# Optimization experiments

Hardware: AMD Instinct MI355X
Metric: run time of the kernel (lower is better)

Reference implementation:

```python
import jax, jax.numpy as jnp
import numpy as np

N_NODES = 100000
N_EDGES = 1600000
D = 128
LN_EPS = 1e-5


def setup_inputs() -> dict:
    key = jax.random.key(0)
    ks = jax.random.split(key, 6)
    return {
        "x": jax.random.normal(ks[0], (N_NODES, D), dtype=jnp.float32),
        "edge_src": jax.random.randint(ks[1], (N_EDGES,), 0, N_NODES, dtype=jnp.int32),
        "edge_dst": jax.random.randint(ks[2], (N_EDGES,), 0, N_NODES, dtype=jnp.int32),
        "edge_val": jax.random.uniform(ks[3], (N_EDGES,), dtype=jnp.float32),
        "w1": jax.random.normal(ks[4], (D,), dtype=jnp.float32),
        "w2": jax.random.normal(ks[5], (D,), dtype=jnp.float32),
        "ln1_g": jnp.ones((D,), dtype=jnp.float32),
        "ln1_b": jnp.zeros((D,), dtype=jnp.float32),
        "ln2_g": jnp.ones((D,), dtype=jnp.float32),
        "ln2_b": jnp.zeros((D,), dtype=jnp.float32),
    }


def _layer_norm(x, g, b):
    mu = jnp.mean(x, axis=-1, keepdims=True)
    var = jnp.mean(jnp.square(x - mu), axis=-1, keepdims=True)
    return (x - mu) * jax.lax.rsqrt(var + LN_EPS) * g + b


def _gat_layer(x, w, src, dst, val, g, b):
    # diag transform: h = x * w  (elementwise over features)
    h = x * w
    # sparse adjacency aggregation: out[dst] += val * h[src]
    msg = val[:, None] * h[src]  # [E, D]
    out = jax.ops.segment_sum(msg, dst, num_segments=x.shape[0])
    return _layer_norm(out, g, b)


def reference(x, edge_src, edge_dst, edge_val, w1, w2, ln1_g, ln1_b, ln2_g, ln2_b):
    # layer 0 (followed by ReLU; dropout is identity in eval mode)
    h = _gat_layer(x, w1, edge_src, edge_dst, edge_val, ln1_g, ln1_b)
    h = jax.nn.relu(h)
    # layer 1 (last layer: no ReLU/dropout)
    out = _gat_layer(h, w2, edge_src, edge_dst, edge_val, ln2_g, ln2_b)
    return out
```

## Files before the change

### kernel.cpp

```cpp
#include <hip/hip_runtime.h>

#define D 128
#define LN_EPS 1e-5f
#define BUCKET_NODES 128
#define BUCKET_SHIFT 7
#define EDGE_CAP 4096
#define FUSE_THREADS 512
#define K2_EPT 16
#define SORT_THREADS 512
#define SORT_EPT 8

__device__ inline unsigned int pack_b2(float a, float b) {
    unsigned ua = __float_as_uint(a);
    unsigned ub = __float_as_uint(b);
    unsigned pa = (ua + 0x7fffu + ((ua >> 16) & 1u)) >> 16;
    unsigned pb = (ub + 0x7fffu + ((ub >> 16) & 1u)) & 0xffff0000u;
    return pa | pb;
}
__device__ inline float lo_b2(unsigned u) { return __uint_as_float((u & 0xffffu) << 16); }
__device__ inline float hi_b2(unsigned u) { return __uint_as_float(u & 0xffff0000u); }

__global__ __launch_bounds__(FUSE_THREADS)
void conv_fill_kernel(const float* __restrict__ x, unsigned int* __restrict__ xb,
                      int nwords, int conv_blocks,
                      const int* __restrict__ src, const int* __restrict__ dst,
                      const float* __restrict__ val,
                      int* __restrict__ gcnt, uint2* __restrict__ edges,
                      int E, int nbuckets) {
    if ((int)blockIdx.x < conv_blocks) {
        int i = blockIdx.x * FUSE_THREADS + threadIdx.x;
        if (i < nwords) {
            int node = i >> 6, f = i & 63;
            xb[i] = pack_b2(x[(size_t)node * D + f], x[(size_t)node * D + 64 + f]);
        }
        return;
    }
    __shared__ int lcnt[1024];
    __shared__ int lbase[1024];
    int fb = (int)blockIdx.x - conv_blocks;
    for (int i = threadIdx.x; i < nbuckets; i += FUSE_THREADS) lcnt[i] = 0;
    __syncthreads();

    int base = fb * (FUSE_THREADS * K2_EPT);
    unsigned int w0[K2_EPT];
    float        w1[K2_EPT];
    int          br[K2_EPT];
    #pragma unroll
    for (int r = 0; r < K2_EPT; ++r) {
        int e = base + r * FUSE_THREADS + threadIdx.x;
        if (e < E) {
            int d = dst[e];
            int b = d >> BUCKET_SHIFT;
            int rk = atomicAdd(&lcnt[b], 1);
            w0[r] = (unsigned)src[e] | ((unsigned)(d & (BUCKET_NODES - 1)) << 20);
            w1[r] = val[e];
            br[r] = (b << 16) | rk;
        } else {
            br[r] = -1;
        }
    }
    __syncthreads();
    for (int i = threadIdx.x; i < nbuckets; i += FUSE_THREADS) {
        int c = lcnt[i];
        lbase[i] = c ? atomicAdd(&gcnt[i], c) : 0;
    }
    __syncthreads();
    #pragma unroll
    for (int r = 0; r < K2_EPT; ++r) {
        if (br[r] >= 0) {
            int b  = br[r] >> 16;
            int rk = br[r] & 0xffff;
            edges[(size_t)b * EDGE_CAP + lbase[b] + rk] =
                make_uint2(w0[r], __float_as_uint(w1[r]));
        }
    }
}

__global__ __launch_bounds__(SORT_THREADS)
void bucket_sort_kernel(uint2* __restrict__ edges,
                        const int* __restrict__ gcnt,
                        int* __restrict__ deg,
                        int* __restrict__ offsets,
                        int N) {
    __shared__ int hist[BUCKET_NODES];
    __shared__ int scan[BUCKET_NODES];
    int b = blockIdx.x;
    int cnt = gcnt[b];
    uint2* ep = edges + (size_t)b * EDGE_CAP;

    if (threadIdx.x < BUCKET_NODES) hist[threadIdx.x] = 0;
    __syncthreads();

    uint2 ed[SORT_EPT];
    int   rk[SORT_EPT];
    int   dl[SORT_EPT];
    #pragma unroll
    for (int r = 0; r < SORT_EPT; ++r) {
        int i = r * SORT_THREADS + threadIdx.x;
        if (i < cnt) {
            uint2 t = ep[i];
            int d = (int)(t.x >> 20);
            ed[r] = t;
            dl[r] = d;
            rk[r] = atomicAdd(&hist[d], 1);
        } else {
            dl[r] = -1;
        }
    }
    __syncthreads();

    if (threadIdx.x < BUCKET_NODES) scan[threadIdx.x] = hist[threadIdx.x];
    __syncthreads();
    #pragma unroll
    for (int off = 1; off < BUCKET_NODES; off <<= 1) {
        int v = 0;
        if (threadIdx.x < BUCKET_NODES && threadIdx.x >= off) v = scan[threadIdx.x - off];
        __syncthreads();
        if (threadIdx.x < BUCKET_NODES) scan[threadIdx.x] += v;
        __syncthreads();
    }

    int node0 = b << BUCKET_SHIFT;
    if (threadIdx.x < BUCKET_NODES) {
        int n = node0 + threadIdx.x;
        if (n < N) {
            deg[n]     = hist[threadIdx.x];
            offsets[n] = b * EDGE_CAP + scan[threadIdx.x] - hist[threadIdx.x];
        }
    }
    __syncthreads();

    #pragma unroll
    for (int r = 0; r < SORT_EPT; ++r) {
        if (dl[r] >= 0) {
            int p = scan[dl[r]] - hist[dl[r]] + rk[r];
            ep[p] = ed[r];
        }
    }
}

__global__ void gather_ln_kernel(const unsigned int* __restrict__ h2,
                                 const int* __restrict__ offsets,
                                 const int* __restrict__ deg,
                                 const uint2* __restrict__ edge_s,
                                 const float* __restrict__ w,
                                 const float* __restrict__ g,
                                 const float* __restrict__ bb,
                                 float* __restrict__ out_f32,
                                 unsigned int* __restrict__ out_b2,
                                 int N, int mode) {
    int node = blockIdx.x * (blockDim.x >> 6) + (threadIdx.x >> 6);
    int lane = threadIdx.x & 63;
    if (node >= N) return;

    int q  = lane >> 4;
    int sl = lane & 15;

    int start = offsets[node];
    int cnt   = deg[node];

    const uint4* h4 = (const uint4*)h2;
    float aA0 = 0.f, aA1 = 0.f, aA2 = 0.f, aA3 = 0.f;
    float aB0 = 0.f, aB1 = 0.f, aB2 = 0.f, aB3 = 0.f;

    for (int base = 0; base < cnt; base += 64) {
        int m = min(64, cnt - base);
        unsigned e0 = 0u, e1 = 0u;
        if (lane < m) { uint2 t = edge_s[start + base + lane]; e0 = t.x; e1 = t.y; }
        for (int j = 0; j < m; j += 4) {
            int idx = j + q;
            int   s = __shfl((int)e0, idx, 64) & 0xfffff;
            float v = __uint_as_float((unsigned)__shfl((int)e1, idx, 64));
            uint4 hw = h4[(size_t)s * 16 + sl];
            aA0 = fmaf(v, lo_b2(hw.x), aA0);  aB0 = fmaf(v, hi_b2(hw.x), aB0);
            aA1 = fmaf(v, lo_b2(hw.y), aA1);  aB1 = fmaf(v, hi_b2(hw.y), aB1);
            aA2 = fmaf(v, lo_b2(hw.z), aA2);  aB2 = fmaf(v, hi_b2(hw.z), aB2);
            aA3 = fmaf(v, lo_b2(hw.w), aA3);  aB3 = fmaf(v, hi_b2(hw.w), aB3);
        }
    }

    aA0 += __shfl_xor(aA0, 16, 64); aA0 += __shfl_xor(aA0, 32, 64);
    aA1 += __shfl_xor(aA1, 16, 64); aA1 += __shfl_xor(aA1, 32, 64);
    aA2 += __shfl_xor(aA2, 16, 64); aA2 += __shfl_xor(aA2, 32, 64);
    aA3 += __shfl_xor(aA3, 16, 64); aA3 += __shfl_xor(aA3, 32, 64);
    aB0 += __shfl_xor(aB0, 16, 64); aB0 += __shfl_xor(aB0, 32, 64);
    aB1 += __shfl_xor(aB1, 16, 64); aB1 += __shfl_xor(aB1, 32, 64);
    aB2 += __shfl_xor(aB2, 16, 64); aB2 += __shfl_xor(aB2, 32, 64);
    aB3 += __shfl_xor(aB3, 16, 64); aB3 += __shfl_xor(aB3, 32, 64);

    float4 wA = ((const float4*)w)[sl];
    float4 wB = ((const float4*)(w + 64))[sl];
    aA0 *= wA.x; aA1 *= wA.y; aA2 *= wA.z; aA3 *= wA.w;
    aB0 *= wB.x; aB1 *= wB.y; aB2 *= wB.z; aB3 *= wB.w;

    float sum = ((aA0 + aA1) + (aA2 + aA3)) + ((aB0 + aB1) + (aB2 + aB3));
    sum += __shfl_xor(sum, 1, 64); sum += __shfl_xor(sum, 2, 64);
    sum += __shfl_xor(sum, 4, 64); sum += __shfl_xor(sum, 8, 64);
    float mu = sum * (1.0f / D);

    float dA0 = aA0 - mu, dA1 = aA1 - mu, dA2 = aA2 - mu, dA3 = aA3 - mu;
    float dB0 = aB0 - mu, dB1 = aB1 - mu, dB2 = aB2 - mu, dB3 = aB3 - mu;
    float sq = ((dA0*dA0 + dA1*dA1) + (dA2*dA2 + dA3*dA3))
             + ((dB0*dB0 + dB1*dB1) + (dB2*dB2 + dB3*dB3));
    sq += __shfl_xor(sq, 1, 64); sq += __shfl_xor(sq, 2, 64);
    sq += __shfl_xor(sq, 4, 64); sq += __shfl_xor(sq, 8, 64);
    float rstd = rsqrtf(sq * (1.0f / D) + LN_EPS);

    float4 gA = ((const float4*)g)[sl];
    float4 gB = ((const float4*)(g + 64))[sl];
    float4 bA = ((const float4*)bb)[sl];
    float4 bB = ((const float4*)(bb + 64))[sl];
    float oA0 = dA0 * rstd * gA.x + bA.x, oA1 = dA1 * rstd * gA.y + bA.y;
    float oA2 = dA2 * rstd * gA.z + bA.z, oA3 = dA3 * rstd * gA.w + bA.w;
    float oB0 = dB0 * rstd * gB.x + bB.x, oB1 = dB1 * rstd * gB.y + bB.y;
    float oB2 = dB2 * rstd * gB.z + bB.z, oB3 = dB3 * rstd * gB.w + bB.w;

    if (mode == 1) {
        oA0 = fmaxf(oA0, 0.f); oA1 = fmaxf(oA1, 0.f);
        oA2 = fmaxf(oA2, 0.f); oA3 = fmaxf(oA3, 0.f);
        oB0 = fmaxf(oB0, 0.f); oB1 = fmaxf(oB1, 0.f);
        oB2 = fmaxf(oB2, 0.f); oB3 = fmaxf(oB3, 0.f);
        if (q == 0) {
            uint4 pw;
            pw.x = pack_b2(oA0, oB0); pw.y = pack_b2(oA1, oB1);
            pw.z = pack_b2(oA2, oB2); pw.w = pack_b2(oA3, oB3);
            ((uint4*)(out_b2 + (size_t)node * 64))[sl] = pw;
        }
    } else {
        if (q == 0) {
            ((float4*)(out_f32 + (size_t)node * D))[sl]      = make_float4(oA0, oA1, oA2, oA3);
            ((float4*)(out_f32 + (size_t)node * D + 64))[sl] = make_float4(oB0, oB1, oB2, oB3);
        }
    }
}

extern "C" void kernel_launch(void* const* d_in, const int* in_sizes, int n_in,
                              void* d_out, int out_size, void* d_ws, size_t ws_size,
                              hipStream_t stream) {
    const float* x    = (const float*)d_in[0];
    const int*   esrc = (const int*)d_in[1];
    const int*   edst = (const int*)d_in[2];
    const float* eval_= (const float*)d_in[3];
    const float* w1   = (const float*)d_in[4];
    const float* w2   = (const float*)d_in[5];
    const float* g1   = (const float*)d_in[6];
    const float* b1   = (const float*)d_in[7];
    const float* g2   = (const float*)d_in[8];
    const float* b2   = (const float*)d_in[9];
    float* out = (float*)d_out;

    const int N = in_sizes[0] / D;
    const int E = in_sizes[1];
    const int nbuckets = (N + BUCKET_NODES - 1) >> BUCKET_SHIFT;

    unsigned int* xb      = (unsigned int*)d_ws;
    unsigned int* hb      = xb + (size_t)N * 64;
    uint2*        edges   = (uint2*)(hb + (size_t)N * 64);
    int*          gcnt    = (int*)(edges + (size_t)nbuckets * EDGE_CAP);
    int*          deg     = gcnt + nbuckets;
    int*          offsets = deg + N;

    const int nwords = N * 64;
    const int conv_blocks = (nwords + FUSE_THREADS - 1) / FUSE_THREADS;
    const int fill_blocks = (E + FUSE_THREADS * K2_EPT - 1) / (FUSE_THREADS * K2_EPT);
    const int ggrid = (N + 3) / 4;

    hipMemsetAsync(gcnt, 0, (size_t)nbuckets * sizeof(int), stream);
    conv_fill_kernel<<<conv_blocks + fill_blocks, FUSE_THREADS, 0, stream>>>(
        x, xb, nwords, conv_blocks, esrc, edst, eval_, gcnt, edges, E, nbuckets);
    bucket_sort_kernel<<<nbuckets, SORT_THREADS, 0, stream>>>(edges, gcnt,
                                                              deg, offsets, N);
    gather_ln_kernel<<<ggrid, 256, 0, stream>>>(xb, offsets, deg, edges,
                                                w1, g1, b1, nullptr, hb, N, 1);
    gather_ln_kernel<<<ggrid, 256, 0, stream>>>(hb, offsets, deg, edges,
                                                w2, g2, b2, out, nullptr, N, 0);
}
```

Before: 308.5 us.

## Fuse bucket sort into gather kernel via LDS sorting, switch to fp16 features

Removes the separate bucket-sort kernel and the deg/offsets arrays. Each gather block now owns one 128-node bucket, sorts that bucket's edges in shared memory, and then has each 16-lane group aggregate whole nodes with two independent loads in flight per iteration. Feature storage moves from bf16 to fp16 packing via cvt_pkrtz. In exchange, the sort is redone in both layers, and 1024-thread blocks with a 32KB LDS buffer may lower occupancy. fp16 also has narrower range than bf16, and cvt_pkrtz rounds toward zero.

```diff
diff --git a/kernel.cpp b/kernel.cpp
--- a/kernel.cpp
+++ b/kernel.cpp
@@ -1,4 +1,6 @@
 #include <hip/hip_runtime.h>
+
+typedef __fp16 half2_t __attribute__((ext_vector_type(2)));
 
 #define D 128
 #define LN_EPS 1e-5f
@@ -7,18 +9,12 @@
 #define EDGE_CAP 4096
 #define FUSE_THREADS 512
 #define K2_EPT 16
-#define SORT_THREADS 512
-#define SORT_EPT 8
-
-__device__ inline unsigned int pack_b2(float a, float b) {
-    unsigned ua = __float_as_uint(a);
-    unsigned ub = __float_as_uint(b);
-    unsigned pa = (ua + 0x7fffu + ((ua >> 16) & 1u)) >> 16;
-    unsigned pb = (ub + 0x7fffu + ((ub >> 16) & 1u)) & 0xffff0000u;
-    return pa | pb;
-}
-__device__ inline float lo_b2(unsigned u) { return __uint_as_float((u & 0xffffu) << 16); }
-__device__ inline float hi_b2(unsigned u) { return __uint_as_float(u & 0xffff0000u); }
+#define GT 1024
+
+__device__ inline unsigned pack_h2(float a, float b) {
+    half2_t p = __builtin_amdgcn_cvt_pkrtz(a, b);
+    return __builtin_bit_cast(unsigned, p);
+}
 
 __global__ __launch_bounds__(FUSE_THREADS)
 void conv_fill_kernel(const float* __restrict__ x, unsigned int* __restrict__ xb,
@@ -31,7 +27,7 @@
         int i = blockIdx.x * FUSE_THREADS + threadIdx.x;
         if (i < nwords) {
             int node = i >> 6, f = i & 63;
-            xb[i] = pack_b2(x[(size_t)node * D + f], x[(size_t)node * D + 64 + f]);
+            xb[i] = pack_h2(x[(size_t)node * D + f], x[(size_t)node * D + 64 + f]);
         }
         return;
     }
@@ -76,160 +72,136 @@
     }
 }
 
-__global__ __launch_bounds__(SORT_THREADS)
-void bucket_sort_kernel(uint2* __restrict__ edges,
-                        const int* __restrict__ gcnt,
-                        int* __restrict__ deg,
-                        int* __restrict__ offsets,
-                        int N) {
+__global__ __launch_bounds__(GT, 8)
+void gather_ln_kernel(const uint4* __restrict__ h4,
+                      const int* __restrict__ gcnt,
+                      const uint2* __restrict__ edges_g,
+                      const float* __restrict__ w,
+                      const float* __restrict__ g,
+                      const float* __restrict__ bb,
+                      float* __restrict__ out_f32,
+                      unsigned int* __restrict__ out_h,
+                      int N, int mode) {
+    __shared__ uint2 eL[EDGE_CAP];
     __shared__ int hist[BUCKET_NODES];
-    __shared__ int scan[BUCKET_NODES];
-    int b = blockIdx.x;
-    int cnt = gcnt[b];
-    uint2* ep = edges + (size_t)b * EDGE_CAP;
-
-    if (threadIdx.x < BUCKET_NODES) hist[threadIdx.x] = 0;
-    __syncthreads();
-
-    uint2 ed[SORT_EPT];
-    int   rk[SORT_EPT];
-    int   dl[SORT_EPT];
-    #pragma unroll
-    for (int r = 0; r < SORT_EPT; ++r) {
-        int i = r * SORT_THREADS + threadIdx.x;
+    __shared__ int scanb[BUCKET_NODES];
+    __shared__ int obase[BUCKET_NODES];
+
+    int bkt = blockIdx.x;
+    int tid = threadIdx.x;
+    int cnt = min(gcnt[bkt], EDGE_CAP);
+    const uint2* ep = edges_g + (size_t)bkt * EDGE_CAP;
+
+    if (tid < BUCKET_NODES) hist[tid] = 0;
+    __syncthreads();
+
+    uint2 ed[4]; int dl[4]; int rk[4];
+    #pragma unroll
+    for (int r = 0; r < 4; ++r) {
+        int i = r * GT + tid;
         if (i < cnt) {
             uint2 t = ep[i];
-            int d = (int)(t.x >> 20);
             ed[r] = t;
-            dl[r] = d;
-            rk[r] = atomicAdd(&hist[d], 1);
-        } else {
-            dl[r] = -1;
-        }
-    }
-    __syncthreads();
-
-    if (threadIdx.x < BUCKET_NODES) scan[threadIdx.x] = hist[threadIdx.x];
+            dl[r] = (int)(t.x >> 20);
+            rk[r] = atomicAdd(&hist[dl[r]], 1);
+        } else dl[r] = -1;
+    }
+    __syncthreads();
+    if (tid < BUCKET_NODES) scanb[tid] = hist[tid];
     __syncthreads();
     #pragma unroll
     for (int off = 1; off < BUCKET_NODES; off <<= 1) {
         int v = 0;
-        if (threadIdx.x < BUCKET_NODES && threadIdx.x >= off) v = scan[threadIdx.x - off];
+        if (tid < BUCKET_NODES && tid >= off) v = scanb[tid - off];
         __syncthreads();
-        if (threadIdx.x < BUCKET_NODES) scan[threadIdx.x] += v;
+        if (tid < BUCKET_NODES) scanb[tid] += v;
         __syncthreads();
     }
-
-    int node0 = b << BUCKET_SHIFT;
-    if (threadIdx.x < BUCKET_NODES) {
-        int n = node0 + threadIdx.x;
-        if (n < N) {
-            deg[n]     = hist[threadIdx.x];
-            offsets[n] = b * EDGE_CAP + scan[threadIdx.x] - hist[threadIdx.x];
-        }
-    }
-    __syncthreads();
-
-    #pragma unroll
-    for (int r = 0; r < SORT_EPT; ++r) {
-        if (dl[r] >= 0) {
-            int p = scan[dl[r]] - hist[dl[r]] + rk[r];
-            ep[p] = ed[r];
-        }
-    }
-}
-
-__global__ void gather_ln_kernel(const unsigned int* __restrict__ h2,
-                                 const int* __restrict__ offsets,
-                                 const int* __restrict__ deg,
-                                 const uint2* __restrict__ edge_s,
-                                 const float* __restrict__ w,
-                                 const float* __restrict__ g,
-                                 const float* __restrict__ bb,
-                                 float* __restrict__ out_f32,
-                                 unsigned int* __restrict__ out_b2,
-                                 int N, int mode) {
-    int node = blockIdx.x * (blockDim.x >> 6) + (threadIdx.x >> 6);
-    int lane = threadIdx.x & 63;
-    if (node >= N) return;
-
-    int q  = lane >> 4;
-    int sl = lane & 15;
-
-    int start = offsets[node];
-    int cnt   = deg[node];
-
-    const uint4* h4 = (const uint4*)h2;
-    float aA0 = 0.f, aA1 = 0.f, aA2 = 0.f, aA3 = 0.f;
-    float aB0 = 0.f, aB1 = 0.f, aB2 = 0.f, aB3 = 0.f;
-
-    for (int base = 0; base < cnt; base += 64) {
-        int m = min(64, cnt - base);
-        unsigned e0 = 0u, e1 = 0u;
-        if (lane < m) { uint2 t = edge_s[start + base + lane]; e0 = t.x; e1 = t.y; }
-        for (int j = 0; j < m; j += 4) {
-            int idx = j + q;
-            int   s = __shfl((int)e0, idx, 64) & 0xfffff;
-            float v = __uint_as_float((unsigned)__shfl((int)e1, idx, 64));
-            uint4 hw = h4[(size_t)s * 16 + sl];
-            aA0 = fmaf(v, lo_b2(hw.x), aA0);  aB0 = fmaf(v, hi_b2(hw.x), aB0);
-            aA1 = fmaf(v, lo_b2(hw.y), aA1);  aB1 = fmaf(v, hi_b2(hw.y), aB1);
-            aA2 = fmaf(v, lo_b2(hw.z), aA2);  aB2 = fmaf(v, hi_b2(hw.z), aB2);
-            aA3 = fmaf(v, lo_b2(hw.w), aA3);  aB3 = fmaf(v, hi_b2(hw.w), aB3);
-        }
-    }
-
-    aA0 += __shfl_xor(aA0, 16, 64); aA0 += __shfl_xor(aA0, 32, 64);
-    aA1 += __shfl_xor(aA1, 16, 64); aA1 += __shfl_xor(aA1, 32, 64);
-    aA2 += __shfl_xor(aA2, 16, 64); aA2 += __shfl_xor(aA2, 32, 64);
-    aA3 += __shfl_xor(aA3, 16, 64); aA3 += __shfl_xor(aA3, 32, 64);
-    aB0 += __shfl_xor(aB0, 16, 64); aB0 += __shfl_xor(aB0, 32, 64);
-    aB1 += __shfl_xor(aB1, 16, 64); aB1 += __shfl_xor(aB1, 32, 64);
-    aB2 += __shfl_xor(aB2, 16, 64); aB2 += __shfl_xor(aB2, 32, 64);
-    aB3 += __shfl_xor(aB3, 16, 64); aB3 += __shfl_xor(aB3, 32, 64);
+    if (tid < BUCKET_NODES) obase[tid] = scanb[tid] - hist[tid];
+    __syncthreads();
+    #pragma unroll
+    for (int r = 0; r < 4; ++r)
+        if (dl[r] >= 0) eL[obase[dl[r]] + rk[r]] = ed[r];
+    __syncthreads();
+
+    int wid = tid >> 6, lane = tid & 63, grp = lane >> 4, sl = lane & 15;
 
     float4 wA = ((const float4*)w)[sl];
     float4 wB = ((const float4*)(w + 64))[sl];
-    aA0 *= wA.x; aA1 *= wA.y; aA2 *= wA.z; aA3 *= wA.w;
-    aB0 *= wB.x; aB1 *= wB.y; aB2 *= wB.z; aB3 *= wB.w;
-
-    float sum = ((aA0 + aA1) + (aA2 + aA3)) + ((aB0 + aB1) + (aB2 + aB3));
-    sum += __shfl_xor(sum, 1, 64); sum += __shfl_xor(sum, 2, 64);
-    sum += __shfl_xor(sum, 4, 64); sum += __shfl_xor(sum, 8, 64);
-    float mu = sum * (1.0f / D);
-
-    float dA0 = aA0 - mu, dA1 = aA1 - mu, dA2 = aA2 - mu, dA3 = aA3 - mu;
-    float dB0 = aB0 - mu, dB1 = aB1 - mu, dB2 = aB2 - mu, dB3 = aB3 - mu;
-    float sq = ((dA0*dA0 + dA1*dA1) + (dA2*dA2 + dA3*dA3))
-             + ((dB0*dB0 + dB1*dB1) + (dB2*dB2 + dB3*dB3));
-    sq += __shfl_xor(sq, 1, 64); sq += __shfl_xor(sq, 2, 64);
-    sq += __shfl_xor(sq, 4, 64); sq += __shfl_xor(sq, 8, 64);
-    float rstd = rsqrtf(sq * (1.0f / D) + LN_EPS);
-
     float4 gA = ((const float4*)g)[sl];
     float4 gB = ((const float4*)(g + 64))[sl];
     float4 bA = ((const float4*)bb)[sl];
     float4 bB = ((const float4*)(bb + 64))[sl];
-    float oA0 = dA0 * rstd * gA.x + bA.x, oA1 = dA1 * rstd * gA.y + bA.y;
-    float oA2 = dA2 * rstd * gA.z + bA.z, oA3 = dA3 * rstd * gA.w + bA.w;
-    float oB0 = dB0 * rstd * gB.x + bB.x, oB1 = dB1 * rstd * gB.y + bB.y;
-    float oB2 = dB2 * rstd * gB.z + bB.z, oB3 = dB3 * rstd * gB.w + bB.w;
-
-    if (mode == 1) {
-        oA0 = fmaxf(oA0, 0.f); oA1 = fmaxf(oA1, 0.f);
-        oA2 = fmaxf(oA2, 0.f); oA3 = fmaxf(oA3, 0.f);
-        oB0 = fmaxf(oB0, 0.f); oB1 = fmaxf(oB1, 0.f);
-        oB2 = fmaxf(oB2, 0.f); oB3 = fmaxf(oB3, 0.f);
-        if (q == 0) {
+
+    #pragma unroll
+    for (int k = 0; k < 2; ++k) {
+        int ni = k * 64 + wid * 4 + grp;
+        int n = (bkt << BUCKET_SHIFT) + ni;
+        if (n >= N) continue;
+        int st = obase[ni], m = hist[ni];
+
+        float aA0=0,aA1=0,aA2=0,aA3=0, aB0=0,aB1=0,aB2=0,aB3=0;
+        for (int j = 0; j < m; j += 2) {
+            uint2 tA = eL[st + j];
+            uint2 tB = (j + 1 < m) ? eL[st + j + 1] : make_uint2(0u, 0u);
+            int   sA = (int)(tA.x & 0xfffffu);
+            float vA = __uint_as_float(tA.y);
+            int   sB = (int)(tB.x & 0xfffffu);
+            float vB = __uint_as_float(tB.y);
+            uint4 hA = h4[(size_t)sA * 16 + sl];
+            uint4 hB = h4[(size_t)sB * 16 + sl];
+            half2_t p;
+            p = __builtin_bit_cast(half2_t, hA.x);
+            aA0 = fmaf(vA, (float)p.x, aA0); aB0 = fmaf(vA, (float)p.y, aB0);
+            p = __builtin_bit_cast(half2_t, hA.y);
+            aA1 = fmaf(vA, (float)p.x, aA1); aB1 = fmaf(vA, (float)p.y, aB1);
+            p = __builtin_bit_cast(half2_t, hA.z);
+            aA2 = fmaf(vA, (float)p.x, aA2); aB2 = fmaf(vA, (float)p.y, aB2);
+            p = __builtin_bit_cast(half2_t, hA.w);
+            aA3 = fmaf(vA, (float)p.x, aA3); aB3 = fmaf(vA, (float)p.y, aB3);
+            p = __builtin_bit_cast(half2_t, hB.x);
+            aA0 = fmaf(vB, (float)p.x, aA0); aB0 = fmaf(vB, (float)p.y, aB0);
+            p = __builtin_bit_cast(half2_t, hB.y);
+            aA1 = fmaf(vB, (float)p.x, aA1); aB1 = fmaf(vB, (float)p.y, aB1);
+            p = __builtin_bit_cast(half2_t, hB.z);
+            aA2 = fmaf(vB, (float)p.x, aA2); aB2 = fmaf(vB, (float)p.y, aB2);
+            p = __builtin_bit_cast(half2_t, hB.w);
+            aA3 = fmaf(vB, (float)p.x, aA3); aB3 = fmaf(vB, (float)p.y, aB3);
+        }
+
+        aA0 *= wA.x; aA1 *= wA.y; aA2 *= wA.z; aA3 *= wA.w;
+        aB0 *= wB.x; aB1 *= wB.y; aB2 *= wB.z; aB3 *= wB.w;
+
+        float sum = ((aA0 + aA1) + (aA2 + aA3)) + ((aB0 + aB1) + (aB2 + aB3));
+        sum += __shfl_xor(sum, 1, 64); sum += __shfl_xor(sum, 2, 64);
+        sum += __shfl_xor(sum, 4, 64); sum += __shfl_xor(sum, 8, 64);
+        float mu = sum * (1.0f / D);
+
+        float dA0 = aA0 - mu, dA1 = aA1 - mu, dA2 = aA2 - mu, dA3 = aA3 - mu;
+        float dB0 = aB0 - mu, dB1 = aB1 - mu, dB2 = aB2 - mu, dB3 = aB3 - mu;
+        float sq = ((dA0*dA0 + dA1*dA1) + (dA2*dA2 + dA3*dA3))
+                 + ((dB0*dB0 + dB1*dB1) + (dB2*dB2 + dB3*dB3));
+        sq += __shfl_xor(sq, 1, 64); sq += __shfl_xor(sq, 2, 64);
+        sq += __shfl_xor(sq, 4, 64); sq += __shfl_xor(sq, 8, 64);
+        float rstd = rsqrtf(sq * (1.0f / D) + LN_EPS);
+
+        float oA0 = dA0 * rstd * gA.x + bA.x, oA1 = dA1 * rstd * gA.y + bA.y;
+        float oA2 = dA2 * rstd * gA.z + bA.z, oA3 = dA3 * rstd * gA.w + bA.w;
+        float oB0 = dB0 * rstd * gB.x + bB.x, oB1 = dB1 * rstd * gB.y + bB.y;
+        float oB2 = dB2 * rstd * gB.z + bB.z, oB3 = dB3 * rstd * gB.w + bB.w;
+
+        if (mode == 1) {
+            oA0 = fmaxf(oA0, 0.f); oA1 = fmaxf(oA1, 0.f);
+            oA2 = fmaxf(oA2, 0.f); oA3 = fmaxf(oA3, 0.f);
+            oB0 = fmaxf(oB0, 0.f); oB1 = fmaxf(oB1, 0.f);
+            oB2 = fmaxf(oB2, 0.f); oB3 = fmaxf(oB3, 0.f);
             uint4 pw;
-            pw.x = pack_b2(oA0, oB0); pw.y = pack_b2(oA1, oB1);
-            pw.z = pack_b2(oA2, oB2); pw.w = pack_b2(oA3, oB3);
-            ((uint4*)(out_b2 + (size_t)node * 64))[sl] = pw;
-        }
-    } else {
-        if (q == 0) {
-            ((float4*)(out_f32 + (size_t)node * D))[sl]      = make_float4(oA0, oA1, oA2, oA3);
-            ((float4*)(out_f32 + (size_t)node * D + 64))[sl] = make_float4(oB0, oB1, oB2, oB3);
+            pw.x = pack_h2(oA0, oB0); pw.y = pack_h2(oA1, oB1);
+            pw.z = pack_h2(oA2, oB2); pw.w = pack_h2(oA3, oB3);
+            ((uint4*)(out_h + (size_t)n * 64))[sl] = pw;
+        } else {
+            ((float4*)(out_f32 + (size_t)n * D))[sl]      = make_float4(oA0, oA1, oA2, oA3);
+            ((float4*)(out_f32 + (size_t)n * D + 64))[sl] = make_float4(oB0, oB1, oB2, oB3);
         }
     }
 }
@@ -253,25 +225,20 @@
     const int E = in_sizes[1];
     const int nbuckets = (N + BUCKET_NODES - 1) >> BUCKET_SHIFT;
 
-    unsigned int* xb      = (unsigned int*)d_ws;
-    unsigned int* hb      = xb + (size_t)N * 64;
-    uint2*        edges   = (uint2*)(hb + (size_t)N * 64);
-    int*          gcnt    = (int*)(edges + (size_t)nbuckets * EDGE_CAP);
-    int*          deg     = gcnt + nbuckets;
-    int*          offsets = deg + N;
+    unsigned int* xb    = (unsigned int*)d_ws;
+    unsigned int* hb    = xb + (size_t)N * 64;
+    uint2*        edges = (uint2*)(hb + (size_t)N * 64);
+    int*          gcnt  = (int*)(edges + (size_t)nbuckets * EDGE_CAP);
 
     const int nwords = N * 64;
     const int conv_blocks = (nwords + FUSE_THREADS - 1) / FUSE_THREADS;
     const int fill_blocks = (E + FUSE_THREADS * K2_EPT - 1) / (FUSE_THREADS * K2_EPT);
-    const int ggrid = (N + 3) / 4;
-
-    hipMemsetAsync(gcnt, 0, (size_t)nbuckets * sizeof(int), stream);
+
+    (void)hipMemsetAsync(gcnt, 0, (size_t)nbuckets * sizeof(int), stream);
     conv_fill_kernel<<<conv_blocks + fill_blocks, FUSE_THREADS, 0, stream>>>(
         x, xb, nwords, conv_blocks, esrc, edst, eval_, gcnt, edges, E, nbuckets);
-    bucket_sort_kernel<<<nbuckets, SORT_THREADS, 0, stream>>>(edges, gcnt,
-                                                              deg, offsets, N);
-    gather_ln_kernel<<<ggrid, 256, 0, stream>>>(xb, offsets, deg, edges,
-                                                w1, g1, b1, nullptr, hb, N, 1);
-    gather_ln_kernel<<<ggrid, 256, 0, stream>>>(hb, offsets, deg, edges,
-                                                w2, g2, b2, out, nullptr, N, 0);
-}
+    gather_ln_kernel<<<nbuckets, GT, 0, stream>>>((const uint4*)xb, gcnt, edges,
+                                                  w1, g1, b1, nullptr, hb, N, 1);
+    gather_ln_kernel<<<nbuckets, GT, 0, stream>>>((const uint4*)hb, gcnt, edges,
+                                                  w2, g2, b2, out, nullptr, N, 0);
+}
```

Result: faster. 295.9 us (-4.1%).
